# Optimization experiments

Measured on AMD Instinct MI355X. Metric: run time of the kernel, lower is better.

Reference implementation:

```python
import jax, jax.numpy as jnp
import numpy as np

N_NODES = 50000
N_EDGES = 800000
D_IN = 128
H1 = 128
H2 = 64
N_CLASSES = 4


def _sage_conv(x, src, dst, w_l, w_r, b, num_nodes):
    # PyG SAGEConv (aggr='mean'): out = lin_l(mean_{j->i} x_j) + lin_r(x_i)
    ones = jnp.ones((src.shape[0],), dtype=x.dtype)
    deg = jax.ops.segment_sum(ones, dst, num_segments=num_nodes)  # [N]
    agg = jax.ops.segment_sum(x[src], dst, num_segments=num_nodes)  # [N, d]
    agg = agg / jnp.maximum(deg, 1.0)[:, None]
    return agg @ w_l + b + x @ w_r


def setup_inputs() -> dict:
    key = jax.random.key(0)
    ks = jax.random.split(key, 12)
    x_content = jax.random.normal(ks[0], (N_NODES, D_IN), dtype=jnp.float32)
    edge_index = jax.random.randint(ks[1], (2, N_EDGES), 0, N_NODES, dtype=jnp.int32)
    edge_type = jax.random.randint(ks[2], (N_EDGES,), 0, 4, dtype=jnp.int32)
    s = 0.05
    params = {
        'w_l0': jax.random.normal(ks[3], (D_IN, H1), jnp.float32) * s,
        'w_r0': jax.random.normal(ks[4], (D_IN, H1), jnp.float32) * s,
        'b0': jnp.zeros((H1,), jnp.float32),
        'w_l1': jax.random.normal(ks[5], (H1, H1), jnp.float32) * s,
        'w_r1': jax.random.normal(ks[6], (H1, H1), jnp.float32) * s,
        'b1': jnp.zeros((H1,), jnp.float32),
        'w_l2': jax.random.normal(ks[7], (H1, H2), jnp.float32) * s,
        'w_r2': jax.random.normal(ks[8], (H1, H2), jnp.float32) * s,
        'b2': jnp.zeros((H2,), jnp.float32),
        'w_out': jax.random.normal(ks[9], (H2, N_CLASSES), jnp.float32) * s,
        'b_out': jnp.zeros((N_CLASSES,), jnp.float32),
    }
    return {'x_content': x_content, 'edge_index': edge_index, 'edge_type': edge_type, **params}


def reference(x_content, edge_index, edge_type,
              w_l0, w_r0, b0, w_l1, w_r1, b1, w_l2, w_r2, b2, w_out, b_out):
    # eval mode: dropout is identity
    src, dst = edge_index[0], edge_index[1]
    n = x_content.shape[0]
    x = x_content
    for (wl, wr, b) in ((w_l0, w_r0, b0), (w_l1, w_r1, b1), (w_l2, w_r2, b2)):
        x = _sage_conv(x, src, dst, wl, wr, b, n)
        x = jax.nn.relu(x)
    return x @ w_out + b_out
```

## Files before the change

kernel.cpp:

```cpp
#include <hip/hip_runtime.h>
#include <hip/hip_fp16.h>

#define D 128

constexpr int SCAN_CHUNK = 1024;
constexpr int NRANGE = 8;
constexpr int NCHUNK = 64;
constexpr int RRC = 6272;

using short8 = __attribute__((ext_vector_type(8))) short;
using f32x4 = __attribute__((ext_vector_type(4))) float;

__device__ inline void splitf(float v, unsigned short& h, unsigned short& l) {
    unsigned b = __float_as_uint(v);
    h = (unsigned short)(b >> 16);
    float fh = __uint_as_float(b & 0xffff0000u);
    float r = v - fh;
    l = (unsigned short)(__float_as_uint(r) >> 16);
}


__global__ __launch_bounds__(1024) void hist_count(
    const int* __restrict__ dst, int* __restrict__ hist,
    int n_edges, int n_nodes, int rr, int ch) {
    __shared__ int lh[RRC];
    int b = blockIdx.x;
    int r = b & (NRANGE - 1), c = b >> 3;
    int t = threadIdx.x;
    for (int i = t; i < rr; i += 1024) lh[i] = 0;
    __syncthreads();
    int lo = r * rr, hi = min(n_nodes, lo + rr);
    int e0 = c * ch, e1 = min(n_edges, e0 + ch);
    for (int e = e0 + t; e < e1; e += 1024) {
        int d = dst[e];
        if (d >= lo && d < hi) atomicAdd(&lh[d - lo], 1);
    }
    __syncthreads();
    int* gh = hist + (size_t)(r * NCHUNK + c) * rr;
    for (int i = t; i < rr; i += 1024) gh[i] = lh[i];
}

__global__ __launch_bounds__(256) void deg_sum(
    const int* __restrict__ hist, int* __restrict__ deg, int n_nodes, int rr) {
    int i = blockIdx.x * 256 + threadIdx.x;
    if (i >= n_nodes) return;
    int r = i / rr, ii = i - r * rr;
    int s = 0;
    for (int c = 0; c < NCHUNK; ++c) s += hist[(size_t)(r * NCHUNK + c) * rr + ii];
    deg[i] = s;
}

__global__ void partial_sums(const int* __restrict__ deg, int* __restrict__ partials, int n) {
    __shared__ int sdata[256];
    int b = blockIdx.x, t = threadIdx.x;
    int base = b * SCAN_CHUNK;
    int sum = 0;
    for (int i = t; i < SCAN_CHUNK; i += 256) {
        int idx = base + i;
        if (idx < n) sum += deg[idx];
    }
    sdata[t] = sum;
    __syncthreads();
    for (int st = 128; st > 0; st >>= 1) {
        if (t < st) sdata[t] += sdata[t + st];
        __syncthreads();
    }
    if (t == 0) partials[b] = sdata[0];
}

__global__ void scan_partials(int* __restrict__ partials, int nb, int* __restrict__ total) {
    if (threadIdx.x == 0 && blockIdx.x == 0) {
        int run = 0;
        for (int i = 0; i < nb; ++i) { int v = partials[i]; partials[i] = run; run += v; }
        *total = run;
    }
}

__global__ void scan_chunks(const int* __restrict__ deg, const int* __restrict__ partials,
                            int* __restrict__ row_ptr, float* __restrict__ inv_deg, int n) {
    __shared__ int soff[256];
    int b = blockIdx.x, t = threadIdx.x;
    int base = b * SCAN_CHUNK;
    int i0 = base + t * 4;
    int v[4];
    int s = 0;
#pragma unroll
    for (int j = 0; j < 4; ++j) {
        int idx = i0 + j;
        v[j] = (idx < n) ? deg[idx] : 0;
        s += v[j];
    }
    soff[t] = s;
    __syncthreads();
    for (int d = 1; d < 256; d <<= 1) {
        int val = (t >= d) ? soff[t - d] : 0;
        __syncthreads();
        soff[t] += val;
        __syncthreads();
    }
    int excl = soff[t] - s + partials[b];
#pragma unroll
    for (int j = 0; j < 4; ++j) {
        int idx = i0 + j;
        if (idx < n) {
            row_ptr[idx] = excl;
            int dv = v[j] > 1 ? v[j] : 1;
            inv_deg[idx] = 1.0f / (float)dv;
            excl += v[j];
        }
    }
}

__global__ __launch_bounds__(256) void base_fill(
    const int* __restrict__ hist, const int* __restrict__ row_ptr,
    int* __restrict__ base, int n_nodes, int rr) {
    int i = blockIdx.x * 256 + threadIdx.x;
    if (i >= n_nodes) return;
    int r = i / rr, ii = i - r * rr;
    int b = row_ptr[i];
    for (int c = 0; c < NCHUNK; ++c) {
        size_t idx = (size_t)(r * NCHUNK + c) * rr + ii;
        base[idx] = b;
        b += hist[idx];
    }
}

__global__ __launch_bounds__(1024) void fill_part(
    const int* __restrict__ src, const int* __restrict__ dst,
    const int* __restrict__ base, int* __restrict__ csr,
    int n_edges, int n_nodes, int rr, int ch) {
    __shared__ int cur[RRC];
    int b = blockIdx.x;
    int r = b & (NRANGE - 1), c = b >> 3;
    int t = threadIdx.x;
    const int* gb = base + (size_t)(r * NCHUNK + c) * rr;
    for (int i = t; i < rr; i += 1024) cur[i] = gb[i];
    __syncthreads();
    int lo = r * rr, hi = min(n_nodes, lo + rr);
    int e0 = c * ch, e1 = min(n_edges, e0 + ch);
    for (int e = e0 + t; e < e1; e += 1024) {
        int d = dst[e];
        if (d >= lo && d < hi) {
            int slot = atomicAdd(&cur[d - lo], 1);
            csr[slot] = src[e];
        }
    }
}

struct WSplitArgs {
    const float* src[6];
    unsigned short* dh[6];
    unsigned short* dl[6];
    int n[6];
};

__global__ __launch_bounds__(256) void split_w(WSplitArgs a) {
    int m = blockIdx.y;
    int N = a.n[m];
    int e = blockIdx.x * 256 + threadIdx.x;
    if (e >= 128 * N) return;
    int sh = (N == 128) ? 7 : 6;
    int k = e >> sh;
    int n = e & (N - 1);
    float v = a.src[m][e];
    unsigned short h, l;
    splitf(v, h, l);
    a.dh[m][n * 128 + k] = h;
    a.dl[m][n * 128 + k] = l;
}

template <int BN, int NT, bool SPLITX>
__global__ __launch_bounds__(256) void gemm_lds(
    const float* __restrict__ X,
    const unsigned short* __restrict__ Ah, const unsigned short* __restrict__ Al,
    const unsigned short* __restrict__ W1h, const unsigned short* __restrict__ W1l,
    const unsigned short* __restrict__ W2h, const unsigned short* __restrict__ W2l,
    const float* __restrict__ bias, __half* __restrict__ P, float* __restrict__ Q, int M) {
    __shared__ short8 As[2][16 * 65];

    const int tid = threadIdx.x;
    const int wave = tid >> 6;
    const int lane = tid & 63;
    const int l15 = lane & 15;
    const int q = lane >> 4;
    const int m0 = blockIdx.x * 64;

    if constexpr (SPLITX) {
#pragma unroll
        for (int it = 0; it < 4; ++it) {
            int s = it * 256 + tid;
            int row = s >> 4, col16 = s & 15;
            int gr = min(m0 + row, M - 1);
            const float4* xp = (const float4*)X + (size_t)gr * 32 + col16 * 2;
            float4 v0 = xp[0], v1 = xp[1];
            float fv[8] = {v0.x, v0.y, v0.z, v0.w, v1.x, v1.y, v1.z, v1.w};
            short8 h, l;
#pragma unroll
            for (int j = 0; j < 8; ++j) {
                unsigned short hh_, ll_;
                splitf(fv[j], hh_, ll_);
                h[j] = (short)hh_;
                l[j] = (short)ll_;
            }
            As[0][col16 * 65 + row] = h;
            As[1][col16 * 65 + row] = l;
        }
    } else {
#pragma unroll
        for (int it = 0; it < 8; ++it) {
            int s = it * 256 + tid;
            int arr = s >> 10;
            int sp = s & 1023;
            int row = sp >> 4, col16 = sp & 15;
            int gr = min(m0 + row, M - 1);
            const unsigned short* src = (arr ? Al : Ah) + (size_t)gr * 128 + col16 * 8;
            As[arr][col16 * 65 + row] = *(const short8*)src;
        }
    }
    __syncthreads();

    const int isQ = wave >> 1;
    const int colbase = (wave & 1) * (NT * 16);
    const unsigned short* Wh = isQ ? W2h : W1h;
    const unsigned short* Wl = isQ ? W2l : W1l;

    float bvs[NT];
#pragma unroll
    for (int nt = 0; nt < NT; ++nt) bvs[nt] = isQ ? bias[colbase + nt * 16 + l15] : 0.f;

    f32x4 acc[4][NT] = {};

#pragma unroll 1
    for (int kt = 0; kt < 4; ++kt) {
        short8 Bh[NT], Bl[NT];
#pragma unroll
        for (int nt = 0; nt < NT; ++nt) {
            int c = colbase + nt * 16 + l15;
            int off = c * 128 + kt * 32 + q * 8;
            Bh[nt] = *(const short8*)(Wh + off);
            Bl[nt] = *(const short8*)(Wl + off);
        }
#pragma unroll
        for (int mt = 0; mt < 4; ++mt) {
            int ai = (kt * 4 + q) * 65 + mt * 16 + l15;
            short8 Afh = As[0][ai];
            short8 Afl = As[1][ai];
#pragma unroll
            for (int nt = 0; nt < NT; ++nt) {
                acc[mt][nt] = __builtin_amdgcn_mfma_f32_16x16x32_bf16(Afh, Bh[nt], acc[mt][nt], 0, 0, 0);
                acc[mt][nt] = __builtin_amdgcn_mfma_f32_16x16x32_bf16(Afh, Bl[nt], acc[mt][nt], 0, 0, 0);
                acc[mt][nt] = __builtin_amdgcn_mfma_f32_16x16x32_bf16(Afl, Bh[nt], acc[mt][nt], 0, 0, 0);
            }
        }
    }

#pragma unroll
    for (int mt = 0; mt < 4; ++mt) {
        int orow = m0 + mt * 16 + q * 4;
#pragma unroll
        for (int nt = 0; nt < NT; ++nt) {
            int col = colbase + nt * 16 + l15;
#pragma unroll
            for (int r = 0; r < 4; ++r) {
                int rr = orow + r;
                if (rr < M) {
                    if (isQ) Q[(size_t)rr * BN + col] = acc[mt][nt][r] + bvs[nt];
                    else P[(size_t)rr * BN + col] = __float2half(acc[mt][nt][r]);
                }
            }
        }
    }
}

__global__ __launch_bounds__(256) void agg_fused128(
    const __half* __restrict__ P, const float* __restrict__ Q,
    const int* __restrict__ row_ptr, const int* __restrict__ csr,
    const float* __restrict__ inv_deg, unsigned short* __restrict__ Hh,
    unsigned short* __restrict__ Hl, int n_nodes) {
    int node = (blockIdx.x * blockDim.x + threadIdx.x) >> 6;
    int lane = threadIdx.x & 63;
    if (node >= n_nodes) return;
    int beg = row_ptr[node], end = row_ptr[node + 1];
    const int half = lane >> 5;
    const int l = lane & 31;
    float a[4][4] = {};
    int e = beg;
    for (; e + 8 <= end; e += 8) {
#pragma unroll
        for (int j = 0; j < 4; ++j) {
            int s = csr[e + 2 * j + half];
            uint2 raw = *(const uint2*)(P + (size_t)s * 128 + l * 4);
            float2 f01 = __half22float2(*reinterpret_cast<__half2*>(&raw.x));
            float2 f23 = __half22float2(*reinterpret_cast<__half2*>(&raw.y));
            a[j][0] += f01.x; a[j][1] += f01.y; a[j][2] += f23.x; a[j][3] += f23.y;
        }
    }
    for (; e < end; e += 2) {
        int idx = e + half;
        if (idx < end) {
            int s = csr[idx];
            uint2 raw = *(const uint2*)(P + (size_t)s * 128 + l * 4);
            float2 f01 = __half22float2(*reinterpret_cast<__half2*>(&raw.x));
            float2 f23 = __half22float2(*reinterpret_cast<__half2*>(&raw.y));
            a[0][0] += f01.x; a[0][1] += f01.y; a[0][2] += f23.x; a[0][3] += f23.y;
        }
    }
    float s0 = (a[0][0] + a[1][0]) + (a[2][0] + a[3][0]);
    float s1 = (a[0][1] + a[1][1]) + (a[2][1] + a[3][1]);
    float s2 = (a[0][2] + a[1][2]) + (a[2][2] + a[3][2]);
    float s3 = (a[0][3] + a[1][3]) + (a[2][3] + a[3][3]);
    s0 += __shfl_xor(s0, 32);
    s1 += __shfl_xor(s1, 32);
    s2 += __shfl_xor(s2, 32);
    s3 += __shfl_xor(s3, 32);
    if (lane < 32) {
        float w = inv_deg[node];
        float4 qv = ((const float4*)Q)[(size_t)node * 32 + l];
        float h0 = fmaxf(fmaf(s0, w, qv.x), 0.f);
        float h1 = fmaxf(fmaf(s1, w, qv.y), 0.f);
        float h2 = fmaxf(fmaf(s2, w, qv.z), 0.f);
        float h3 = fmaxf(fmaf(s3, w, qv.w), 0.f);
        ushort4 hv, lv;
        splitf(h0, hv.x, lv.x);
        splitf(h1, hv.y, lv.y);
        splitf(h2, hv.z, lv.z);
        splitf(h3, hv.w, lv.w);
        ((ushort4*)Hh)[(size_t)node * 32 + l] = hv;
        ((ushort4*)Hl)[(size_t)node * 32 + l] = lv;
    }
}

__global__ __launch_bounds__(256) void agg64_head(
    const __half* __restrict__ P, const float* __restrict__ Q,
    const int* __restrict__ row_ptr, const int* __restrict__ csr,
    const float* __restrict__ inv_deg, const float* __restrict__ Wo,
    const float* __restrict__ bo, float* __restrict__ out, int n_nodes) {
    int node = (blockIdx.x * blockDim.x + threadIdx.x) >> 6;
    int lane = threadIdx.x & 63;
    if (node >= n_nodes) return;
    int beg = row_ptr[node], end = row_ptr[node + 1];
    const int quarter = lane >> 4;
    const int l = lane & 15;
    float a[2][4] = {};
    int e = beg;
    for (; e + 8 <= end; e += 8) {
#pragma unroll
        for (int j = 0; j < 2; ++j) {
            int s = csr[e + 4 * j + quarter];
            uint2 raw = *(const uint2*)(P + (size_t)s * 64 + l * 4);
            float2 f01 = __half22float2(*reinterpret_cast<__half2*>(&raw.x));
            float2 f23 = __half22float2(*reinterpret_cast<__half2*>(&raw.y));
            a[j][0] += f01.x; a[j][1] += f01.y; a[j][2] += f23.x; a[j][3] += f23.y;
        }
    }
    for (; e < end; e += 4) {
        int idx = e + quarter;
        if (idx < end) {
            int s = csr[idx];
            uint2 raw = *(const uint2*)(P + (size_t)s * 64 + l * 4);
            float2 f01 = __half22float2(*reinterpret_cast<__half2*>(&raw.x));
            float2 f23 = __half22float2(*reinterpret_cast<__half2*>(&raw.y));
            a[0][0] += f01.x; a[0][1] += f01.y; a[0][2] += f23.x; a[0][3] += f23.y;
        }
    }
    float s0 = a[0][0] + a[1][0];
    float s1 = a[0][1] + a[1][1];
    float s2 = a[0][2] + a[1][2];
    float s3 = a[0][3] + a[1][3];
    s0 += __shfl_xor(s0, 16); s0 += __shfl_xor(s0, 32);
    s1 += __shfl_xor(s1, 16); s1 += __shfl_xor(s1, 32);
    s2 += __shfl_xor(s2, 16); s2 += __shfl_xor(s2, 32);
    s3 += __shfl_xor(s3, 16); s3 += __shfl_xor(s3, 32);
    if (lane < 16) {
        float w = inv_deg[node];
        float4 qv = ((const float4*)Q)[(size_t)node * 16 + l];
        float h0 = fmaxf(fmaf(s0, w, qv.x), 0.f);
        float h1 = fmaxf(fmaf(s1, w, qv.y), 0.f);
        float h2 = fmaxf(fmaf(s2, w, qv.z), 0.f);
        float h3 = fmaxf(fmaf(s3, w, qv.w), 0.f);
        const float4* Wo4 = (const float4*)Wo;
        float4 w0 = Wo4[4 * l + 0], w1 = Wo4[4 * l + 1], w2 = Wo4[4 * l + 2], w3 = Wo4[4 * l + 3];
        float c0 = h0 * w0.x + h1 * w1.x + h2 * w2.x + h3 * w3.x;
        float c1 = h0 * w0.y + h1 * w1.y + h2 * w2.y + h3 * w3.y;
        float c2 = h0 * w0.z + h1 * w1.z + h2 * w2.z + h3 * w3.z;
        float c3 = h0 * w0.w + h1 * w1.w + h2 * w2.w + h3 * w3.w;
#pragma unroll
        for (int m = 8; m > 0; m >>= 1) {
            c0 += __shfl_xor(c0, m);
            c1 += __shfl_xor(c1, m);
            c2 += __shfl_xor(c2, m);
            c3 += __shfl_xor(c3, m);
        }
        if (l == 0) {
            float4 r;
            r.x = c0 + bo[0];
            r.y = c1 + bo[1];
            r.z = c2 + bo[2];
            r.w = c3 + bo[3];
            ((float4*)out)[node] = r;
        }
    }
}

extern "C" void kernel_launch(void* const* d_in, const int* in_sizes, int n_in,
                              void* d_out, int out_size, void* d_ws, size_t ws_size,
                              hipStream_t stream) {
    const float* x = (const float*)d_in[0];
    const int* ei = (const int*)d_in[1];
    const float* wl0 = (const float*)d_in[3];
    const float* wr0 = (const float*)d_in[4];
    const float* b0 = (const float*)d_in[5];
    const float* wl1 = (const float*)d_in[6];
    const float* wr1 = (const float*)d_in[7];
    const float* b1 = (const float*)d_in[8];
    const float* wl2 = (const float*)d_in[9];
    const float* wr2 = (const float*)d_in[10];
    const float* b2 = (const float*)d_in[11];
    const float* wo = (const float*)d_in[12];
    const float* bo = (const float*)d_in[13];

    const int n_nodes = in_sizes[0] / D;
    const int n_edges = in_sizes[1] / 2;
    const int* srcp = ei;
    const int* dstp = ei + n_edges;

    char* ws = (char*)d_ws;
    size_t off = 0;
    auto carve = [&](size_t bytes) -> void* {
        void* p = ws + off;
        off = (off + bytes + 255) & ~(size_t)255;
        return p;
    };
    int* deg = (int*)carve((size_t)n_nodes * 4);
    int* row_ptr = (int*)carve((size_t)(n_nodes + 1) * 4);
    int* partials = (int*)carve(256 * 4);
    float* inv_deg = (float*)carve((size_t)n_nodes * 4);
    int* csr = (int*)carve((size_t)n_edges * 4);
    __half* Pbuf = (__half*)carve((size_t)n_nodes * D * 2);
    float* Qbuf = (float*)carve((size_t)n_nodes * D * 4);
    unsigned short* hh = (unsigned short*)carve((size_t)n_nodes * D * 2);
    unsigned short* hl = (unsigned short*)carve((size_t)n_nodes * D * 2);
    unsigned short* wt = (unsigned short*)carve((size_t)(4 * 128 * 128 + 2 * 64 * 128) * 2 * 2);
    unsigned short* wl0h = wt;
    unsigned short* wl0l = wl0h + 128 * 128;
    unsigned short* wr0h = wl0l + 128 * 128;
    unsigned short* wr0l = wr0h + 128 * 128;
    unsigned short* wl1h = wr0l + 128 * 128;
    unsigned short* wl1l = wl1h + 128 * 128;
    unsigned short* wr1h = wl1l + 128 * 128;
    unsigned short* wr1l = wr1h + 128 * 128;
    unsigned short* wl2h = wr1l + 128 * 128;
    unsigned short* wl2l = wl2h + 64 * 128;
    unsigned short* wr2h = wl2l + 64 * 128;
    unsigned short* wr2l = wr2h + 64 * 128;

    const int rr = (n_nodes + NRANGE - 1) / NRANGE;
    const int ch = (n_edges + NCHUNK - 1) / NCHUNK;
    int* hist = (int*)Qbuf;
    int* basep = (int*)Pbuf;

    const int nchunk_scan = (n_nodes + SCAN_CHUNK - 1) / SCAN_CHUNK;

    hist_count<<<NRANGE * NCHUNK, 1024, 0, stream>>>(dstp, hist, n_edges, n_nodes, rr, ch);
    deg_sum<<<(n_nodes + 255) / 256, 256, 0, stream>>>(hist, deg, n_nodes, rr);
    partial_sums<<<nchunk_scan, 256, 0, stream>>>(deg, partials, n_nodes);
    scan_partials<<<1, 64, 0, stream>>>(partials, nchunk_scan, row_ptr + n_nodes);
    scan_chunks<<<nchunk_scan, 256, 0, stream>>>(deg, partials, row_ptr, inv_deg, n_nodes);
    base_fill<<<(n_nodes + 255) / 256, 256, 0, stream>>>(hist, row_ptr, basep, n_nodes, rr);
    fill_part<<<NRANGE * NCHUNK, 1024, 0, stream>>>(srcp, dstp, basep, csr, n_edges, n_nodes, rr, ch);

    WSplitArgs wa;
    wa.src[0] = wl0; wa.dh[0] = wl0h; wa.dl[0] = wl0l; wa.n[0] = 128;
    wa.src[1] = wr0; wa.dh[1] = wr0h; wa.dl[1] = wr0l; wa.n[1] = 128;
    wa.src[2] = wl1; wa.dh[2] = wl1h; wa.dl[2] = wl1l; wa.n[2] = 128;
    wa.src[3] = wr1; wa.dh[3] = wr1h; wa.dl[3] = wr1l; wa.n[3] = 128;
    wa.src[4] = wl2; wa.dh[4] = wl2h; wa.dl[4] = wl2l; wa.n[4] = 64;
    wa.src[5] = wr2; wa.dh[5] = wr2h; wa.dl[5] = wr2l; wa.n[5] = 64;
    split_w<<<dim3(64, 6), 256, 0, stream>>>(wa);

    const int agg_blocks = (n_nodes * 64 + 255) / 256;
    const int gemm_blocks = (n_nodes + 63) / 64;

    gemm_lds<128, 4, true><<<gemm_blocks, 256, 0, stream>>>(
        x, nullptr, nullptr, wl0h, wl0l, wr0h, wr0l, b0, Pbuf, Qbuf, n_nodes);
    agg_fused128<<<agg_blocks, 256, 0, stream>>>(Pbuf, Qbuf, row_ptr, csr, inv_deg, hh, hl, n_nodes);
    gemm_lds<128, 4, false><<<gemm_blocks, 256, 0, stream>>>(
        nullptr, hh, hl, wl1h, wl1l, wr1h, wr1l, b1, Pbuf, Qbuf, n_nodes);
    agg_fused128<<<agg_blocks, 256, 0, stream>>>(Pbuf, Qbuf, row_ptr, csr, inv_deg, hh, hl, n_nodes);
    gemm_lds<64, 2, false><<<gemm_blocks, 256, 0, stream>>>(
        nullptr, hh, hl, wl2h, wl2l, wr2h, wr2l, b2, Pbuf, Qbuf, n_nodes);
    agg64_head<<<agg_blocks, 256, 0, stream>>>(Pbuf, Qbuf, row_ptr, csr, inv_deg,
                                               wo, bo, (float*)d_out, n_nodes);
}
```

Baseline: 320.6 us.

## Fuse CSR build scan kernels and widen per-lane loads in 128-d aggregation

Result: faster. 306.7 us (-4.3%).

```diff
diff --git a/kernel.cpp b/kernel.cpp
--- a/kernel.cpp
+++ b/kernel.cpp
@@ -3,9 +3,8 @@
 
 #define D 128
 
-constexpr int SCAN_CHUNK = 1024;
 constexpr int NRANGE = 8;
-constexpr int NCHUNK = 64;
+constexpr int NCHUNK = 32;
 constexpr int RRC = 6272;
 
 using short8 = __attribute__((ext_vector_type(8))) short;
@@ -40,88 +39,67 @@
     for (int i = t; i < rr; i += 1024) gh[i] = lh[i];
 }
 
-__global__ __launch_bounds__(256) void deg_sum(
-    const int* __restrict__ hist, int* __restrict__ deg, int n_nodes, int rr) {
-    int i = blockIdx.x * 256 + threadIdx.x;
-    if (i >= n_nodes) return;
-    int r = i / rr, ii = i - r * rr;
+__global__ __launch_bounds__(256) void deg_sum_partials(
+    const int* __restrict__ hist, int* __restrict__ deg,
+    int* __restrict__ partials, int n_nodes, int rr) {
+    __shared__ int sd[256];
+    int b = blockIdx.x, t = threadIdx.x;
+    int i = b * 256 + t;
     int s = 0;
-    for (int c = 0; c < NCHUNK; ++c) s += hist[(size_t)(r * NCHUNK + c) * rr + ii];
-    deg[i] = s;
-}
-
-__global__ void partial_sums(const int* __restrict__ deg, int* __restrict__ partials, int n) {
-    __shared__ int sdata[256];
+    if (i < n_nodes) {
+        int r = i / rr, ii = i - r * rr;
+        for (int c = 0; c < NCHUNK; ++c) s += hist[(size_t)(r * NCHUNK + c) * rr + ii];
+        deg[i] = s;
+    }
+    sd[t] = s;
+    __syncthreads();
+    for (int st = 128; st > 0; st >>= 1) {
+        if (t < st) sd[t] += sd[t + st];
+        __syncthreads();
+    }
+    if (t == 0) partials[b] = sd[0];
+}
+
+__global__ __launch_bounds__(256) void scan_fill(
+    const int* __restrict__ deg, const int* __restrict__ partials,
+    const int* __restrict__ hist, int* __restrict__ row_ptr,
+    float* __restrict__ inv_deg, int* __restrict__ base,
+    int n_nodes, int rr, int nblk) {
+    __shared__ int sp[256];
+    __shared__ int sd[256];
     int b = blockIdx.x, t = threadIdx.x;
-    int base = b * SCAN_CHUNK;
-    int sum = 0;
-    for (int i = t; i < SCAN_CHUNK; i += 256) {
-        int idx = base + i;
-        if (idx < n) sum += deg[idx];
-    }
-    sdata[t] = sum;
+
+    sp[t] = (t < b && t < nblk) ? partials[t] : 0;
     __syncthreads();
     for (int st = 128; st > 0; st >>= 1) {
-        if (t < st) sdata[t] += sdata[t + st];
+        if (t < st) sp[t] += sp[t + st];
         __syncthreads();
     }
-    if (t == 0) partials[b] = sdata[0];
-}
-
-__global__ void scan_partials(int* __restrict__ partials, int nb, int* __restrict__ total) {
-    if (threadIdx.x == 0 && blockIdx.x == 0) {
-        int run = 0;
-        for (int i = 0; i < nb; ++i) { int v = partials[i]; partials[i] = run; run += v; }
-        *total = run;
-    }
-}
-
-__global__ void scan_chunks(const int* __restrict__ deg, const int* __restrict__ partials,
-                            int* __restrict__ row_ptr, float* __restrict__ inv_deg, int n) {
-    __shared__ int soff[256];
-    int b = blockIdx.x, t = threadIdx.x;
-    int base = b * SCAN_CHUNK;
-    int i0 = base + t * 4;
-    int v[4];
-    int s = 0;
-#pragma unroll
-    for (int j = 0; j < 4; ++j) {
-        int idx = i0 + j;
-        v[j] = (idx < n) ? deg[idx] : 0;
-        s += v[j];
-    }
-    soff[t] = s;
+    int pbase = sp[0];
+
+    int i = b * 256 + t;
+    int v = (i < n_nodes) ? deg[i] : 0;
+    sd[t] = v;
     __syncthreads();
     for (int d = 1; d < 256; d <<= 1) {
-        int val = (t >= d) ? soff[t - d] : 0;
+        int x = (t >= d) ? sd[t - d] : 0;
         __syncthreads();
-        soff[t] += val;
+        sd[t] += x;
         __syncthreads();
     }
-    int excl = soff[t] - s + partials[b];
-#pragma unroll
-    for (int j = 0; j < 4; ++j) {
-        int idx = i0 + j;
-        if (idx < n) {
-            row_ptr[idx] = excl;
-            int dv = v[j] > 1 ? v[j] : 1;
-            inv_deg[idx] = 1.0f / (float)dv;
-            excl += v[j];
-        }
-    }
-}
-
-__global__ __launch_bounds__(256) void base_fill(
-    const int* __restrict__ hist, const int* __restrict__ row_ptr,
-    int* __restrict__ base, int n_nodes, int rr) {
-    int i = blockIdx.x * 256 + threadIdx.x;
-    if (i >= n_nodes) return;
-    int r = i / rr, ii = i - r * rr;
-    int b = row_ptr[i];
-    for (int c = 0; c < NCHUNK; ++c) {
-        size_t idx = (size_t)(r * NCHUNK + c) * rr + ii;
-        base[idx] = b;
-        b += hist[idx];
+    int excl = sd[t] - v + pbase;
+    if (i < n_nodes) {
+        row_ptr[i] = excl;
+        int dv = v > 1 ? v : 1;
+        inv_deg[i] = 1.0f / (float)dv;
+        if (i == n_nodes - 1) row_ptr[n_nodes] = excl + v;
+        int r = i / rr, ii = i - r * rr;
+        int bacc = excl;
+        for (int c = 0; c < NCHUNK; ++c) {
+            size_t idx = (size_t)(r * NCHUNK + c) * rr + ii;
+            base[idx] = bacc;
+            bacc += hist[idx];
+        }
     }
 }
 
@@ -281,52 +259,69 @@
     int lane = threadIdx.x & 63;
     if (node >= n_nodes) return;
     int beg = row_ptr[node], end = row_ptr[node + 1];
-    const int half = lane >> 5;
-    const int l = lane & 31;
-    float a[4][4] = {};
+    const int g = lane >> 4;
+    const int l = lane & 15;
+    float a[2][8] = {};
     int e = beg;
     for (; e + 8 <= end; e += 8) {
 #pragma unroll
-        for (int j = 0; j < 4; ++j) {
-            int s = csr[e + 2 * j + half];
-            uint2 raw = *(const uint2*)(P + (size_t)s * 128 + l * 4);
+        for (int j = 0; j < 2; ++j) {
+            int s = csr[e + 4 * j + g];
+            uint4 raw = *(const uint4*)(P + (size_t)s * 128 + l * 8);
             float2 f01 = __half22float2(*reinterpret_cast<__half2*>(&raw.x));
             float2 f23 = __half22float2(*reinterpret_cast<__half2*>(&raw.y));
+            float2 f45 = __half22float2(*reinterpret_cast<__half2*>(&raw.z));
+            float2 f67 = __half22float2(*reinterpret_cast<__half2*>(&raw.w));
             a[j][0] += f01.x; a[j][1] += f01.y; a[j][2] += f23.x; a[j][3] += f23.y;
-        }
-    }
-    for (; e < end; e += 2) {
-        int idx = e + half;
+            a[j][4] += f45.x; a[j][5] += f45.y; a[j][6] += f67.x; a[j][7] += f67.y;
+        }
+    }
+    for (; e < end; e += 4) {
+        int idx = e + g;
         if (idx < end) {
             int s = csr[idx];
-            uint2 raw = *(const uint2*)(P + (size_t)s * 128 + l * 4);
+            uint4 raw = *(const uint4*)(P + (size_t)s * 128 + l * 8);
             float2 f01 = __half22float2(*reinterpret_cast<__half2*>(&raw.x));
             float2 f23 = __half22float2(*reinterpret_cast<__half2*>(&raw.y));
+            float2 f45 = __half22float2(*reinterpret_cast<__half2*>(&raw.z));
+            float2 f67 = __half22float2(*reinterpret_cast<__half2*>(&raw.w));
             a[0][0] += f01.x; a[0][1] += f01.y; a[0][2] += f23.x; a[0][3] += f23.y;
-        }
-    }
-    float s0 = (a[0][0] + a[1][0]) + (a[2][0] + a[3][0]);
-    float s1 = (a[0][1] + a[1][1]) + (a[2][1] + a[3][1]);
-    float s2 = (a[0][2] + a[1][2]) + (a[2][2] + a[3][2]);
-    float s3 = (a[0][3] + a[1][3]) + (a[2][3] + a[3][3]);
-    s0 += __shfl_xor(s0, 32);
-    s1 += __shfl_xor(s1, 32);
-    s2 += __shfl_xor(s2, 32);
-    s3 += __shfl_xor(s3, 32);
-    if (lane < 32) {
+            a[0][4] += f45.x; a[0][5] += f45.y; a[0][6] += f67.x; a[0][7] += f67.y;
+        }
+    }
+    float s[8];
+#pragma unroll
+    for (int k = 0; k < 8; ++k) {
+        s[k] = a[0][k] + a[1][k];
+        s[k] += __shfl_xor(s[k], 16);
+        s[k] += __shfl_xor(s[k], 32);
+    }
+    if (lane < 16) {
         float w = inv_deg[node];
-        float4 qv = ((const float4*)Q)[(size_t)node * 32 + l];
-        float h0 = fmaxf(fmaf(s0, w, qv.x), 0.f);
-        float h1 = fmaxf(fmaf(s1, w, qv.y), 0.f);
-        float h2 = fmaxf(fmaf(s2, w, qv.z), 0.f);
-        float h3 = fmaxf(fmaf(s3, w, qv.w), 0.f);
-        ushort4 hv, lv;
-        splitf(h0, hv.x, lv.x);
-        splitf(h1, hv.y, lv.y);
-        splitf(h2, hv.z, lv.z);
-        splitf(h3, hv.w, lv.w);
-        ((ushort4*)Hh)[(size_t)node * 32 + l] = hv;
-        ((ushort4*)Hl)[(size_t)node * 32 + l] = lv;
+        const float4* Q4 = (const float4*)Q;
+        float4 q0 = Q4[(size_t)node * 32 + 2 * l];
+        float4 q1 = Q4[(size_t)node * 32 + 2 * l + 1];
+        float h0 = fmaxf(fmaf(s[0], w, q0.x), 0.f);
+        float h1 = fmaxf(fmaf(s[1], w, q0.y), 0.f);
+        float h2 = fmaxf(fmaf(s[2], w, q0.z), 0.f);
+        float h3 = fmaxf(fmaf(s[3], w, q0.w), 0.f);
+        float h4 = fmaxf(fmaf(s[4], w, q1.x), 0.f);
+        float h5 = fmaxf(fmaf(s[5], w, q1.y), 0.f);
+        float h6 = fmaxf(fmaf(s[6], w, q1.z), 0.f);
+        float h7 = fmaxf(fmaf(s[7], w, q1.w), 0.f);
+        ushort4 hv0, lv0, hv1, lv1;
+        splitf(h0, hv0.x, lv0.x);
+        splitf(h1, hv0.y, lv0.y);
+        splitf(h2, hv0.z, lv0.z);
+        splitf(h3, hv0.w, lv0.w);
+        splitf(h4, hv1.x, lv1.x);
+        splitf(h5, hv1.y, lv1.y);
+        splitf(h6, hv1.z, lv1.z);
+        splitf(h7, hv1.w, lv1.w);
+        ((ushort4*)Hh)[(size_t)node * 32 + 2 * l] = hv0;
+        ((ushort4*)Hh)[(size_t)node * 32 + 2 * l + 1] = hv1;
+        ((ushort4*)Hl)[(size_t)node * 32 + 2 * l] = lv0;
+        ((ushort4*)Hl)[(size_t)node * 32 + 2 * l + 1] = lv1;
     }
 }
 
@@ -459,14 +454,11 @@
     int* hist = (int*)Qbuf;
     int* basep = (int*)Pbuf;
 
-    const int nchunk_scan = (n_nodes + SCAN_CHUNK - 1) / SCAN_CHUNK;
+    const int nblk = (n_nodes + 255) / 256;
 
     hist_count<<<NRANGE * NCHUNK, 1024, 0, stream>>>(dstp, hist, n_edges, n_nodes, rr, ch);
-    deg_sum<<<(n_nodes + 255) / 256, 256, 0, stream>>>(hist, deg, n_nodes, rr);
-    partial_sums<<<nchunk_scan, 256, 0, stream>>>(deg, partials, n_nodes);
-    scan_partials<<<1, 64, 0, stream>>>(partials, nchunk_scan, row_ptr + n_nodes);
-    scan_chunks<<<nchunk_scan, 256, 0, stream>>>(deg, partials, row_ptr, inv_deg, n_nodes);
-    base_fill<<<(n_nodes + 255) / 256, 256, 0, stream>>>(hist, row_ptr, basep, n_nodes, rr);
+    deg_sum_partials<<<nblk, 256, 0, stream>>>(hist, deg, partials, n_nodes, rr);
+    scan_fill<<<nblk, 256, 0, stream>>>(deg, partials, hist, row_ptr, inv_deg, basep, n_nodes, rr, nblk);
     fill_part<<<NRANGE * NCHUNK, 1024, 0, stream>>>(srcp, dstp, basep, csr, n_edges, n_nodes, rr, ch);
 
     WSplitArgs wa;
```
